# Kernel optimization log

Measured on AMD Instinct MI355X. Metric: run time of the kernel, lower is better.

Reference implementation:

```python
import jax, jax.numpy as jnp
import numpy as np

B, C, H, W = 8, 512, 32, 32
EMB, HEADS, GROUPS = 512, 8, 32
DH = EMB // HEADS
EPS = 1e-5


def setup_inputs() -> dict:
    key = jax.random.key(0)
    ks = jax.random.split(key, 11)
    s_in = 1.0 / np.sqrt(C)
    s_emb = 1.0 / np.sqrt(EMB)
    return {
        "x": jax.random.normal(ks[0], (B, C, H, W), jnp.float32),
        "Wq": jax.random.uniform(ks[1], (C, EMB), jnp.float32, -s_in, s_in),
        "bq": jax.random.uniform(ks[2], (EMB,), jnp.float32, -s_in, s_in),
        "Wk": jax.random.uniform(ks[3], (C, EMB), jnp.float32, -s_in, s_in),
        "bk": jax.random.uniform(ks[4], (EMB,), jnp.float32, -s_in, s_in),
        "Wv": jax.random.uniform(ks[5], (C, EMB), jnp.float32, -s_in, s_in),
        "bv": jax.random.uniform(ks[6], (EMB,), jnp.float32, -s_in, s_in),
        "Wo": jax.random.uniform(ks[7], (EMB, EMB), jnp.float32, -s_emb, s_emb),
        "bo": jax.random.uniform(ks[8], (EMB,), jnp.float32, -s_emb, s_emb),
        "gn_w": jnp.ones((EMB,), jnp.float32),
        "gn_b": jnp.zeros((EMB,), jnp.float32),
    }


def _group_norm(y, w, b):
    # y: [B, C, H, W]; normalize within each of GROUPS channel groups over (C//G, H, W)
    b_, c_, h_, w_ = y.shape
    yg = y.reshape(b_, GROUPS, c_ // GROUPS, h_, w_)
    mean = yg.mean(axis=(2, 3, 4), keepdims=True)
    var = yg.var(axis=(2, 3, 4), keepdims=True)
    yg = (yg - mean) * jax.lax.rsqrt(var + EPS)
    y = yg.reshape(b_, c_, h_, w_)
    return y * w[None, :, None, None] + b[None, :, None, None]


def reference(x, Wq, bq, Wk, bk, Wv, bv, Wo, bo, gn_w, gn_b):
    b, c, h, w = x.shape
    s = h * w
    xs = x.reshape(b, c, s).transpose(0, 2, 1)  # [B, S, C]
    # QKV projections, split into heads: [B, heads, S, dh]
    def heads(t):
        return t.reshape(b, s, HEADS, DH).transpose(0, 2, 1, 3)
    q = heads(xs @ Wq + bq)
    k = heads(xs @ Wk + bk)
    v = heads(xs @ Wv + bv)
    scale = DH ** -0.5
    scores = jnp.einsum('bhqd,bhkd->bhqk', q, k) * scale  # [B, heads, S, S]
    attn = jax.nn.softmax(scores, axis=-1)
    out = jnp.einsum('bhqk,bhkd->bhqd', attn, v)  # [B, heads, S, dh]
    out = out.transpose(0, 2, 1, 3).reshape(b, s, EMB)  # concat heads
    proj = out @ Wo + bo  # [B, S, EMB]
    proj = proj.transpose(0, 2, 1).reshape(b, EMB, h, w)
    return _group_norm(proj + x, gn_w, gn_b)
```

## Files before the change

kernel.cpp:

```cpp
#include <hip/hip_runtime.h>

#define BB 8
#define CC 512
#define SS 1024
#define EMB 512
#define HEADS 8
#define DH 64
#define GROUPS 32
#define CPG 16
#define EPS 1e-5f

typedef __bf16 bf16x8 __attribute__((ext_vector_type(8)));
typedef __bf16 bf16x4 __attribute__((ext_vector_type(4)));
typedef float f32x4 __attribute__((ext_vector_type(4)));
typedef unsigned short u16x4 __attribute__((ext_vector_type(4)));

__device__ inline unsigned short f2bf(float f) {
    union { float f; unsigned u; } c; c.f = f;
    unsigned u = c.u + 0x7FFF + ((c.u >> 16) & 1);
    return (unsigned short)(u >> 16);
}

#if defined(__has_builtin)
#if __has_builtin(__builtin_amdgcn_exp2f)
#define EXP2F(x) __builtin_amdgcn_exp2f(x)
#endif
#endif
#ifndef EXP2F
#define EXP2F(x) __expf(0.69314718f * (x))
#endif

#define MFMA16(a, b, c) __builtin_amdgcn_mfma_f32_16x16x32_bf16((a), (b), (c), 0, 0, 0)
#define GLOAD_LDS16(g, s)                                                     \
    __builtin_amdgcn_global_load_lds(                                         \
        (const __attribute__((address_space(1))) void*)(g),                   \
        (__attribute__((address_space(3))) void*)(s), 16, 0, 0)

__global__ __launch_bounds__(256) void prep_all(
    const float* __restrict__ x,
    const float* __restrict__ Wq, const float* __restrict__ Wk,
    const float* __restrict__ Wv, const float* __restrict__ Wo,
    unsigned short* __restrict__ xT, unsigned short* __restrict__ Wt)
{
    __shared__ float tile[32][33];
    const int t = threadIdx.x;

    if (blockIdx.x < 4096) {
        const int i  = blockIdx.x;
        const int s0 = (i & 31) * 32;
        const int c0 = ((i >> 5) & 15) * 32;
        const int b  = i >> 9;
        {
            int c = t >> 3, s4 = (t & 7) * 4;
            float4 v = *(const float4*)(x + ((size_t)b * CC + c0 + c) * SS + s0 + s4);
            tile[c][s4] = v.x; tile[c][s4 + 1] = v.y;
            tile[c][s4 + 2] = v.z; tile[c][s4 + 3] = v.w;
        }
        __syncthreads();
        {
            int sr = t >> 3, c4 = (t & 7) * 4;
            u16x4 o;
            #pragma unroll
            for (int i2 = 0; i2 < 4; ++i2) o[i2] = f2bf(tile[c4 + i2][sr]);
            *(u16x4*)(xT + ((size_t)(b << 10) + s0 + sr) * CC + c0 + c4) = o;
        }
    } else {
        const int i  = blockIdx.x - 4096;
        const int k0 = (i & 15) * 32;
        const int n0 = ((i >> 4) & 15) * 32;
        const int z  = i >> 8;
        const float* W = (z == 0) ? Wq : (z == 1) ? Wk : (z == 2) ? Wv : Wo;
        unsigned short* dst = Wt + (size_t)z * EMB * CC;
        {
            int k = t >> 3, n4 = (t & 7) * 4;
            float4 v = *(const float4*)(W + (size_t)(k0 + k) * EMB + n0 + n4);
            tile[k][n4] = v.x; tile[k][n4 + 1] = v.y;
            tile[k][n4 + 2] = v.z; tile[k][n4 + 3] = v.w;
        }
        __syncthreads();
        {
            int n = t >> 3, k4 = (t & 7) * 4;
            u16x4 o;
            #pragma unroll
            for (int i2 = 0; i2 < 4; ++i2) o[i2] = f2bf(tile[k4 + i2][n]);
            *(u16x4*)(dst + (size_t)(n0 + n) * CC + k0 + k4) = o;
        }
    }
}

#define GEMM_CORE(Aptr, Bptr)                                                  \
    __shared__ __align__(16) char lds[32768];                                  \
    const int t = threadIdx.x, w = t >> 6, l = t & 63;                         \
    const int wr = w >> 1, wc = w & 1;                                         \
    const int rl = l & 15, kh = l >> 4;                                        \
    f32x4 acc[4][4] = {};                                                      \
    {                                                                          \
        const int srow = w * 32 + (l >> 2);                                    \
        const int sslot = (l & 3) ^ ((srow >> 1) & 3);                         \
        const char* Ag0 = (const char*)(Aptr) + (size_t)(m0 + srow) * 1024 + sslot * 16;      \
        const char* Ag1 = (const char*)(Aptr) + (size_t)(m0 + srow + 16) * 1024 + (((l & 3) ^ (((srow + 16) >> 1) & 3)) * 16); \
        const char* Bg0 = (const char*)(Bptr) + (size_t)(n0 + srow) * 1024 + sslot * 16;      \
        const char* Bg1 = (const char*)(Bptr) + (size_t)(n0 + srow + 16) * 1024 + (((l & 3) ^ (((srow + 16) >> 1) & 3)) * 16); \
        for (int kt = 0; kt < 16; ++kt) {                                      \
            if (kt == 0) {                                                     \
                GLOAD_LDS16(Ag0, lds + w * 2048);                              \
                GLOAD_LDS16(Ag1, lds + w * 2048 + 1024);                       \
                GLOAD_LDS16(Bg0, lds + 8192 + w * 2048);                       \
                GLOAD_LDS16(Bg1, lds + 8192 + w * 2048 + 1024);                \
                __syncthreads();                                               \
            }                                                                  \
            const int buf = kt & 1;                                            \
            if (kt < 15) {                                                     \
                const int kb = (kt + 1) * 64;                                  \
                char* Al = lds + (buf ^ 1) * 16384;                            \
                char* Bl = Al + 8192;                                          \
                GLOAD_LDS16(Ag0 + kb, Al + w * 2048);                          \
                GLOAD_LDS16(Ag1 + kb, Al + w * 2048 + 1024);                   \
                GLOAD_LDS16(Bg0 + kb, Bl + w * 2048);                          \
                GLOAD_LDS16(Bg1 + kb, Bl + w * 2048 + 1024);                   \
            }                                                                  \
            const char* Al = lds + buf * 16384;                                \
            const char* Bl = Al + 8192;                                        \
            bf16x8 af[4], bfr[4];                                              \
            _Pragma("unroll")                                                  \
            for (int i = 0; i < 4; ++i) {                                      \
                int row = wr * 64 + i * 16 + rl;                               \
                af[i] = *(const bf16x8*)(Al + row * 64 + ((kh ^ ((row >> 1) & 3)) << 4)); \
                int col = wc * 64 + i * 16 + rl;                               \
                bfr[i] = *(const bf16x8*)(Bl + col * 64 + ((kh ^ ((col >> 1) & 3)) << 4)); \
            }                                                                  \
            _Pragma("unroll")                                                  \
            for (int i = 0; i < 4; ++i)                                        \
                _Pragma("unroll")                                              \
                for (int j = 0; j < 4; ++j)                                    \
                    acc[i][j] = MFMA16(af[i], bfr[j], acc[i][j]);              \
            __syncthreads();                                                   \
        }                                                                      \
    }

__global__ __launch_bounds__(256) void qkv_mm(
    const unsigned short* __restrict__ xT, const unsigned short* __restrict__ Wt,
    const float* __restrict__ bq, const float* __restrict__ bk,
    const float* __restrict__ bv,
    unsigned short* __restrict__ Qb, unsigned short* __restrict__ Kb,
    unsigned short* __restrict__ Vb)
{
    const int z = blockIdx.z;
    const unsigned short* Bt = Wt + (size_t)z * EMB * CC;
    const float* bias = (z == 0) ? bq : (z == 1) ? bk : bv;
    const int m0 = blockIdx.x * 128, n0 = blockIdx.y * 128;

    GEMM_CORE(xT, Bt)

    if (z == 2) {
        #pragma unroll
        for (int i = 0; i < 4; ++i) {
            #pragma unroll
            for (int j = 0; j < 4; ++j) {
                int n = n0 + wc * 64 + j * 16 + rl;
                int h = n >> 6, d = n & 63;
                float bi = bias[n];
                int mb = m0 + wr * 64 + i * 16 + kh * 4;
                int b = mb >> 10, s = mb & 1023;
                bf16x4 o;
                #pragma unroll
                for (int r = 0; r < 4; ++r) o[r] = (__bf16)(acc[i][j][r] + bi);
                *(bf16x4*)((__bf16*)Vb + (((size_t)(b * HEADS + h)) * DH + d) * SS + s) = o;
            }
        }
    } else {
        unsigned short* outp = (z == 0) ? Qb : Kb;
        const float qs = (z == 0) ? 0.1803368801f : 1.0f;
        #pragma unroll
        for (int i = 0; i < 4; ++i) {
            #pragma unroll
            for (int j = 0; j < 4; ++j) {
                int n = n0 + wc * 64 + j * 16 + rl;
                int h = n >> 6, d = n & 63;
                float bi = bias[n];
                #pragma unroll
                for (int r = 0; r < 4; ++r) {
                    int m = m0 + wr * 64 + i * 16 + kh * 4 + r;
                    int b = m >> 10, s = m & 1023;
                    ((__bf16*)outp)[(((size_t)(b * HEADS + h)) * SS + s) * DH + d] =
                        (__bf16)((acc[i][j][r] + bi) * qs);
                }
            }
        }
    }
}

__global__ __launch_bounds__(256) void proj_mm(
    const unsigned short* __restrict__ AO, const unsigned short* __restrict__ Wot,
    const float* __restrict__ bo, const float* __restrict__ x,
    unsigned short* __restrict__ Yb)
{
    const int m0 = blockIdx.x * 128, n0 = blockIdx.y * 128;

    GEMM_CORE(AO, Wot)

    #pragma unroll
    for (int i = 0; i < 4; ++i) {
        #pragma unroll
        for (int j = 0; j < 4; ++j) {
            int n = n0 + wc * 64 + j * 16 + rl;
            float bi = bo[n];
            int mb = m0 + wr * 64 + i * 16 + kh * 4;
            int b = mb >> 10, s = mb & 1023;
            const float4 xr = *(const float4*)(x + ((size_t)b * CC + n) * SS + s);
            bf16x4 o;
            o[0] = (__bf16)(acc[i][j][0] + bi + xr.x);
            o[1] = (__bf16)(acc[i][j][1] + bi + xr.y);
            o[2] = (__bf16)(acc[i][j][2] + bi + xr.z);
            o[3] = (__bf16)(acc[i][j][3] + bi + xr.w);
            *(bf16x4*)((__bf16*)Yb + ((size_t)b * CC + n) * SS + s) = o;
        }
    }
}

__global__ __launch_bounds__(256) void attn_mfma(
    const unsigned short* __restrict__ Q, const unsigned short* __restrict__ K,
    const unsigned short* __restrict__ V, unsigned short* __restrict__ Aout)
{
    __shared__ __align__(16) char lds[49152];

    const int wg  = blockIdx.x;
    const int xcd = wg & 7;
    const int idx = wg >> 3;
    const int pair = xcd * 8 + (idx >> 3);
    const int qb   = idx & 7;
    const int h = pair & 7;
    const int b = pair >> 3;
    const int q0 = qb * 128;

    const size_t kbase = ((size_t)b * HEADS + h) * SS * DH;
    const size_t vbase = ((size_t)b * HEADS + h) * DH * SS;

    const int t  = threadIdx.x;
    const int w  = t >> 6;
    const int l  = t & 63;
    const int g  = l >> 4;
    const int qi = l & 15;
    char* Pl = lds + 32768 + w * 4096;

    bf16x8 qf[2][2];
    #pragma unroll
    for (int u = 0; u < 2; ++u) {
        const unsigned short* qrow =
            Q + kbase + (size_t)(q0 + w * 32 + u * 16 + qi) * DH;
        qf[u][0] = *(const bf16x8*)(qrow + g * 8);
        qf[u][1] = *(const bf16x8*)(qrow + 32 + g * 8);
    }

    const int srow = t >> 3;
    const int seg  = t & 7;
    const unsigned short* kg0 = K + kbase + (size_t)srow * DH + ((seg ^ (srow & 7)) * 8);
    const unsigned short* vg0 = V + vbase + (size_t)srow * SS + ((seg ^ (srow & 7)) * 8);

#define ATTN_STAGE(bb, ktn)                                                    \
    GLOAD_LDS16(kg0 + (ktn) * 4096, lds + (bb) + t * 16);                      \
    GLOAD_LDS16(kg0 + (ktn) * 4096 + 2048, lds + (bb) + 4096 + t * 16);        \
    GLOAD_LDS16(vg0 + (ktn) * 64, lds + (bb) + 8192 + t * 16);                 \
    GLOAD_LDS16(vg0 + (ktn) * 64 + 32768, lds + (bb) + 12288 + t * 16);

    f32x4 O[4][2] = {};
    float m2[2]   = {-1e30f, -1e30f};
    float lsum[2] = {0.f, 0.f};

    int bufb = 0;
    ATTN_STAGE(0, 0)
    __syncthreads();

    for (int kt = 0; kt < 16; ++kt) {
        if (kt < 15) { ATTN_STAGE(bufb ^ 16384, kt + 1) }

        const char* Kl = lds + bufb;
        const char* Vl = lds + bufb + 8192;

        f32x4 st[4][2] = {};
        __builtin_amdgcn_s_setprio(1);
        #pragma unroll
        for (int tt = 0; tt < 4; ++tt) {
            int row = tt * 16 + qi;
            bf16x8 kf0 = *(const bf16x8*)(Kl + row * 128 +
                          ((g * 16) ^ ((row & 7) << 4)));
            bf16x8 kf1 = *(const bf16x8*)(Kl + row * 128 +
                          ((64 + g * 16) ^ ((row & 7) << 4)));
            #pragma unroll
            for (int u = 0; u < 2; ++u) {
                st[tt][u] = MFMA16(kf0, qf[u][0], st[tt][u]);
                st[tt][u] = MFMA16(kf1, qf[u][1], st[tt][u]);
            }
        }
        __builtin_amdgcn_s_setprio(0);

        float pmax[2] = {-1e30f, -1e30f};
        #pragma unroll
        for (int tt = 0; tt < 4; ++tt)
            #pragma unroll
            for (int u = 0; u < 2; ++u)
                #pragma unroll
                for (int r = 0; r < 4; ++r)
                    pmax[u] = fmaxf(pmax[u], st[tt][u][r]);
        #pragma unroll
        for (int u = 0; u < 2; ++u) {
            if (!__all(pmax[u] <= m2[u] + 8.0f)) {
                float gm = fmaxf(pmax[u], __shfl_xor(pmax[u], 16));
                gm = fmaxf(gm, __shfl_xor(gm, 32));
                float newm = fmaxf(m2[u], gm);
                float alpha = EXP2F(m2[u] - newm);
                #pragma unroll
                for (int dt = 0; dt < 4; ++dt)
                    #pragma unroll
                    for (int r = 0; r < 4; ++r) O[dt][u][r] *= alpha;
                lsum[u] *= alpha;
                m2[u] = newm;
            }
            #pragma unroll
            for (int tt = 0; tt < 4; ++tt) {
                bf16x4 pk;
                #pragma unroll
                for (int r = 0; r < 4; ++r) {
                    float p = EXP2F(st[tt][u][r] - m2[u]);
                    lsum[u] += p;
                    pk[r] = (__bf16)p;
                }
                *(bf16x4*)(Pl + u * 2048 + qi * 128 +
                           ((tt * 32 + g * 8) ^ ((qi & 7) << 4))) = pk;
            }
        }

        bf16x8 pf[2][2];
        #pragma unroll
        for (int u = 0; u < 2; ++u)
            #pragma unroll
            for (int hh = 0; hh < 2; ++hh)
                pf[u][hh] = *(const bf16x8*)(Pl + u * 2048 + qi * 128 +
                             ((hh * 64 + g * 16) ^ ((qi & 7) << 4)));
        __builtin_amdgcn_s_setprio(1);
        #pragma unroll
        for (int dt = 0; dt < 4; ++dt) {
            int d = dt * 16 + qi;
            bf16x8 vf0 = *(const bf16x8*)(Vl + d * 128 + ((g * 16) ^ ((d & 7) << 4)));
            bf16x8 vf1 = *(const bf16x8*)(Vl + d * 128 + ((64 + g * 16) ^ ((d & 7) << 4)));
            #pragma unroll
            for (int u = 0; u < 2; ++u) {
                O[dt][u] = MFMA16(vf0, pf[u][0], O[dt][u]);
                O[dt][u] = MFMA16(vf1, pf[u][1], O[dt][u]);
            }
        }
        __builtin_amdgcn_s_setprio(0);

        __syncthreads();
        bufb ^= 16384;
    }

    #pragma unroll
    for (int u = 0; u < 2; ++u) {
        float ls = lsum[u];
        ls += __shfl_xor(ls, 16);
        ls += __shfl_xor(ls, 32);
        const float inv = __builtin_amdgcn_rcpf(ls);
        unsigned short* orow = Aout +
            ((size_t)b * SS + q0 + w * 32 + u * 16 + qi) * EMB + h * DH;
        #pragma unroll
        for (int dt = 0; dt < 4; ++dt) {
            bf16x4 o;
            #pragma unroll
            for (int r = 0; r < 4; ++r) o[r] = (__bf16)(O[dt][u][r] * inv);
            *(bf16x4*)((__bf16*)orow + dt * 16 + g * 4) = o;
        }
    }
#undef ATTN_STAGE
}

__global__ __launch_bounds__(256) void gnorm3(
    const __bf16* __restrict__ Yb, const float* __restrict__ gw,
    const float* __restrict__ gb, float* __restrict__ out)
{
    __shared__ __align__(16) __bf16 ybuf[CPG * SS];
    __shared__ float red[8];
    __shared__ float stats[2];

    const int grp = blockIdx.x;
    const int b   = blockIdx.y;
    const int t   = threadIdx.x;
    const size_t base = ((size_t)b * CC + grp * CPG) * SS;
    const __bf16* src = Yb + base;

    float sum = 0.f, sq = 0.f;
    #pragma unroll
    for (int i = 0; i < 8; ++i) {
        int off = i * 2048 + t * 8;
        bf16x8 v = *(const bf16x8*)(src + off);
        *(bf16x8*)(ybuf + off) = v;
        #pragma unroll
        for (int j = 0; j < 8; ++j) {
            float f = (float)v[j];
            sum += f; sq += f * f;
        }
    }
    #pragma unroll
    for (int off = 32; off; off >>= 1) {
        sum += __shfl_down(sum, off);
        sq  += __shfl_down(sq, off);
    }
    const int wid = t >> 6;
    if ((t & 63) == 0) { red[wid] = sum; red[4 + wid] = sq; }
    __syncthreads();
    if (t == 0) {
        float s1 = red[0] + red[1] + red[2] + red[3];
        float s2 = red[4] + red[5] + red[6] + red[7];
        float mean = s1 / (float)(CPG * SS);
        float var  = s2 / (float)(CPG * SS) - mean * mean;
        stats[0] = mean;
        stats[1] = rsqrtf(var + EPS);
    }
    __syncthreads();
    const float mean = stats[0], rs = stats[1];

    #pragma unroll
    for (int i = 0; i < 8; ++i) {
        int off = i * 2048 + t * 8;
        int ch = grp * CPG + (off >> 10);
        float wgt = gw[ch] * rs, bet = gb[ch] - mean * rs * gw[ch];
        bf16x8 v = *(const bf16x8*)(ybuf + off);
        float4 o0, o1;
        o0.x = (float)v[0] * wgt + bet; o0.y = (float)v[1] * wgt + bet;
        o0.z = (float)v[2] * wgt + bet; o0.w = (float)v[3] * wgt + bet;
        o1.x = (float)v[4] * wgt + bet; o1.y = (float)v[5] * wgt + bet;
        o1.z = (float)v[6] * wgt + bet; o1.w = (float)v[7] * wgt + bet;
        *(float4*)(out + base + off)     = o0;
        *(float4*)(out + base + off + 4) = o1;
    }
}

extern "C" void kernel_launch(void* const* d_in, const int* in_sizes, int n_in,
                              void* d_out, int out_size, void* d_ws, size_t ws_size,
                              hipStream_t stream) {
    const float* x   = (const float*)d_in[0];
    const float* Wq  = (const float*)d_in[1];
    const float* bq  = (const float*)d_in[2];
    const float* Wk  = (const float*)d_in[3];
    const float* bk  = (const float*)d_in[4];
    const float* Wv  = (const float*)d_in[5];
    const float* bv  = (const float*)d_in[6];
    const float* Wo  = (const float*)d_in[7];
    const float* bo  = (const float*)d_in[8];
    const float* gnw = (const float*)d_in[9];
    const float* gnb = (const float*)d_in[10];
    float* out = (float*)d_out;
    char* ws  = (char*)d_ws;

    unsigned short* xT  = (unsigned short*)(ws);
    unsigned short* Wt  = (unsigned short*)(ws + 8388608);
    unsigned short* Qb  = (unsigned short*)(ws + 10485760);
    unsigned short* Kb  = (unsigned short*)(ws + 18874368);
    unsigned short* Vb  = (unsigned short*)(ws + 27262976);
    unsigned short* AO  = (unsigned short*)(ws + 35651584);
    unsigned short* Yb  = (unsigned short*)(ws + 44040192);

    prep_all<<<dim3(5120), 256, 0, stream>>>(x, Wq, Wk, Wv, Wo, xT, Wt);
    qkv_mm<<<dim3(64, 4, 3), 256, 0, stream>>>(xT, Wt, bq, bk, bv, Qb, Kb, Vb);
    attn_mfma<<<dim3(512), 256, 0, stream>>>(Qb, Kb, Vb, AO);
    proj_mm<<<dim3(64, 4), 256, 0, stream>>>(AO, Wt + (size_t)3 * EMB * CC, bo, x, Yb);
    gnorm3<<<dim3(32, 8), 256, 0, stream>>>((const __bf16*)Yb, gnw, gnb, out);
}
```

Measured before the change: 83.18 us.

## Load K/V fragments directly from global memory and halve attention query tile

The attention kernel drops its double-buffered LDS staging of K and V tiles and block-wide barriers. Each wave now loads its K and V MFMA fragments straight from global memory, leaving LDS only for the per-wave P tile. The query tile per block shrinks from 128 to 64 rows, with 16 per wave, and the grid doubles to 1024 blocks. This cuts LDS use and sync overhead and should raise occupancy, but it loses K/V reuse across waves through LDS, so global and L2 traffic for K/V roughly quadruples and there is no explicit prefetch overlap.

Result: slower. 168.9 us (+103.1%).

```diff
diff --git a/kernel.cpp b/kernel.cpp
--- a/kernel.cpp
+++ b/kernel.cpp
@@ -222,16 +222,16 @@
     const unsigned short* __restrict__ Q, const unsigned short* __restrict__ K,
     const unsigned short* __restrict__ V, unsigned short* __restrict__ Aout)
 {
-    __shared__ __align__(16) char lds[49152];
+    __shared__ __align__(16) char lds[8192];
 
     const int wg  = blockIdx.x;
     const int xcd = wg & 7;
     const int idx = wg >> 3;
-    const int pair = xcd * 8 + (idx >> 3);
-    const int qb   = idx & 7;
+    const int pair = xcd * 8 + (idx >> 4);
+    const int qb   = idx & 15;
     const int h = pair & 7;
     const int b = pair >> 3;
-    const int q0 = qb * 128;
+    const int q0 = qb * 64;
 
     const size_t kbase = ((size_t)b * HEADS + h) * SS * DH;
     const size_t vbase = ((size_t)b * HEADS + h) * DH * SS;
@@ -241,137 +241,96 @@
     const int l  = t & 63;
     const int g  = l >> 4;
     const int qi = l & 15;
-    char* Pl = lds + 32768 + w * 4096;
-
-    bf16x8 qf[2][2];
+    char* Pl = lds + w * 2048;
+
+    bf16x8 qf[2];
+    {
+        const unsigned short* qrow = Q + kbase + (size_t)(q0 + w * 16 + qi) * DH;
+        qf[0] = *(const bf16x8*)(qrow + g * 8);
+        qf[1] = *(const bf16x8*)(qrow + 32 + g * 8);
+    }
+
+    f32x4 O[4] = {};
+    float m2 = -1e30f, lsum = 0.f;
+
+    #pragma unroll 1
+    for (int kt = 0; kt < 16; ++kt) {
+        const unsigned short* kp = K + kbase + (size_t)(kt * 64 + qi) * DH + g * 8;
+        bf16x8 kf[4][2];
+        #pragma unroll
+        for (int tt = 0; tt < 4; ++tt) {
+            kf[tt][0] = *(const bf16x8*)(kp + tt * 16 * DH);
+            kf[tt][1] = *(const bf16x8*)(kp + tt * 16 * DH + 32);
+        }
+        const unsigned short* vp = V + vbase + (size_t)qi * SS + kt * 64 + g * 8;
+        bf16x8 vf[4][2];
+        #pragma unroll
+        for (int dt = 0; dt < 4; ++dt) {
+            vf[dt][0] = *(const bf16x8*)(vp + (size_t)(dt * 16) * SS);
+            vf[dt][1] = *(const bf16x8*)(vp + (size_t)(dt * 16) * SS + 32);
+        }
+
+        f32x4 st[4] = {};
+        __builtin_amdgcn_s_setprio(1);
+        #pragma unroll
+        for (int tt = 0; tt < 4; ++tt) {
+            st[tt] = MFMA16(kf[tt][0], qf[0], st[tt]);
+            st[tt] = MFMA16(kf[tt][1], qf[1], st[tt]);
+        }
+        __builtin_amdgcn_s_setprio(0);
+
+        float pmax = -1e30f;
+        #pragma unroll
+        for (int tt = 0; tt < 4; ++tt)
+            #pragma unroll
+            for (int r = 0; r < 4; ++r)
+                pmax = fmaxf(pmax, st[tt][r]);
+        if (!__all(pmax <= m2 + 8.0f)) {
+            float gm = fmaxf(pmax, __shfl_xor(pmax, 16));
+            gm = fmaxf(gm, __shfl_xor(gm, 32));
+            float newm = fmaxf(m2, gm);
+            float alpha = EXP2F(m2 - newm);
+            #pragma unroll
+            for (int dt = 0; dt < 4; ++dt)
+                #pragma unroll
+                for (int r = 0; r < 4; ++r) O[dt][r] *= alpha;
+            lsum *= alpha;
+            m2 = newm;
+        }
+        #pragma unroll
+        for (int tt = 0; tt < 4; ++tt) {
+            bf16x4 pk;
+            #pragma unroll
+            for (int r = 0; r < 4; ++r) {
+                float p = EXP2F(st[tt][r] - m2);
+                lsum += p;
+                pk[r] = (__bf16)p;
+            }
+            *(bf16x4*)(Pl + qi * 128 + ((tt * 32 + g * 8) ^ ((qi & 7) << 4))) = pk;
+        }
+
+        bf16x8 pf0 = *(const bf16x8*)(Pl + qi * 128 + ((g * 16) ^ ((qi & 7) << 4)));
+        bf16x8 pf1 = *(const bf16x8*)(Pl + qi * 128 + ((64 + g * 16) ^ ((qi & 7) << 4)));
+        __builtin_amdgcn_s_setprio(1);
+        #pragma unroll
+        for (int dt = 0; dt < 4; ++dt) {
+            O[dt] = MFMA16(vf[dt][0], pf0, O[dt]);
+            O[dt] = MFMA16(vf[dt][1], pf1, O[dt]);
+        }
+        __builtin_amdgcn_s_setprio(0);
+    }
+
+    lsum += __shfl_xor(lsum, 16);
+    lsum += __shfl_xor(lsum, 32);
+    const float inv = __builtin_amdgcn_rcpf(lsum);
+    unsigned short* orow = Aout + ((size_t)b * SS + q0 + w * 16 + qi) * EMB + h * DH;
     #pragma unroll
-    for (int u = 0; u < 2; ++u) {
-        const unsigned short* qrow =
-            Q + kbase + (size_t)(q0 + w * 32 + u * 16 + qi) * DH;
-        qf[u][0] = *(const bf16x8*)(qrow + g * 8);
-        qf[u][1] = *(const bf16x8*)(qrow + 32 + g * 8);
-    }
-
-    const int srow = t >> 3;
-    const int seg  = t & 7;
-    const unsigned short* kg0 = K + kbase + (size_t)srow * DH + ((seg ^ (srow & 7)) * 8);
-    const unsigned short* vg0 = V + vbase + (size_t)srow * SS + ((seg ^ (srow & 7)) * 8);
-
-#define ATTN_STAGE(bb, ktn)                                                    \
-    GLOAD_LDS16(kg0 + (ktn) * 4096, lds + (bb) + t * 16);                      \
-    GLOAD_LDS16(kg0 + (ktn) * 4096 + 2048, lds + (bb) + 4096 + t * 16);        \
-    GLOAD_LDS16(vg0 + (ktn) * 64, lds + (bb) + 8192 + t * 16);                 \
-    GLOAD_LDS16(vg0 + (ktn) * 64 + 32768, lds + (bb) + 12288 + t * 16);
-
-    f32x4 O[4][2] = {};
-    float m2[2]   = {-1e30f, -1e30f};
-    float lsum[2] = {0.f, 0.f};
-
-    int bufb = 0;
-    ATTN_STAGE(0, 0)
-    __syncthreads();
-
-    for (int kt = 0; kt < 16; ++kt) {
-        if (kt < 15) { ATTN_STAGE(bufb ^ 16384, kt + 1) }
-
-        const char* Kl = lds + bufb;
-        const char* Vl = lds + bufb + 8192;
-
-        f32x4 st[4][2] = {};
-        __builtin_amdgcn_s_setprio(1);
-        #pragma unroll
-        for (int tt = 0; tt < 4; ++tt) {
-            int row = tt * 16 + qi;
-            bf16x8 kf0 = *(const bf16x8*)(Kl + row * 128 +
-                          ((g * 16) ^ ((row & 7) << 4)));
-            bf16x8 kf1 = *(const bf16x8*)(Kl + row * 128 +
-                          ((64 + g * 16) ^ ((row & 7) << 4)));
-            #pragma unroll
-            for (int u = 0; u < 2; ++u) {
-                st[tt][u] = MFMA16(kf0, qf[u][0], st[tt][u]);
-                st[tt][u] = MFMA16(kf1, qf[u][1], st[tt][u]);
-            }
-        }
-        __builtin_amdgcn_s_setprio(0);
-
-        float pmax[2] = {-1e30f, -1e30f};
-        #pragma unroll
-        for (int tt = 0; tt < 4; ++tt)
-            #pragma unroll
-            for (int u = 0; u < 2; ++u)
-                #pragma unroll
-                for (int r = 0; r < 4; ++r)
-                    pmax[u] = fmaxf(pmax[u], st[tt][u][r]);
-        #pragma unroll
-        for (int u = 0; u < 2; ++u) {
-            if (!__all(pmax[u] <= m2[u] + 8.0f)) {
-                float gm = fmaxf(pmax[u], __shfl_xor(pmax[u], 16));
-                gm = fmaxf(gm, __shfl_xor(gm, 32));
-                float newm = fmaxf(m2[u], gm);
-                float alpha = EXP2F(m2[u] - newm);
-                #pragma unroll
-                for (int dt = 0; dt < 4; ++dt)
-                    #pragma unroll
-                    for (int r = 0; r < 4; ++r) O[dt][u][r] *= alpha;
-                lsum[u] *= alpha;
-                m2[u] = newm;
-            }
-            #pragma unroll
-            for (int tt = 0; tt < 4; ++tt) {
-                bf16x4 pk;
-                #pragma unroll
-                for (int r = 0; r < 4; ++r) {
-                    float p = EXP2F(st[tt][u][r] - m2[u]);
-                    lsum[u] += p;
-                    pk[r] = (__bf16)p;
-                }
-                *(bf16x4*)(Pl + u * 2048 + qi * 128 +
-                           ((tt * 32 + g * 8) ^ ((qi & 7) << 4))) = pk;
-            }
-        }
-
-        bf16x8 pf[2][2];
-        #pragma unroll
-        for (int u = 0; u < 2; ++u)
-            #pragma unroll
-            for (int hh = 0; hh < 2; ++hh)
-                pf[u][hh] = *(const bf16x8*)(Pl + u * 2048 + qi * 128 +
-                             ((hh * 64 + g * 16) ^ ((qi & 7) << 4)));
-        __builtin_amdgcn_s_setprio(1);
-        #pragma unroll
-        for (int dt = 0; dt < 4; ++dt) {
-            int d = dt * 16 + qi;
-            bf16x8 vf0 = *(const bf16x8*)(Vl + d * 128 + ((g * 16) ^ ((d & 7) << 4)));
-            bf16x8 vf1 = *(const bf16x8*)(Vl + d * 128 + ((64 + g * 16) ^ ((d & 7) << 4)));
-            #pragma unroll
-            for (int u = 0; u < 2; ++u) {
-                O[dt][u] = MFMA16(vf0, pf[u][0], O[dt][u]);
-                O[dt][u] = MFMA16(vf1, pf[u][1], O[dt][u]);
-            }
-        }
-        __builtin_amdgcn_s_setprio(0);
-
-        __syncthreads();
-        bufb ^= 16384;
-    }
-
-    #pragma unroll
-    for (int u = 0; u < 2; ++u) {
-        float ls = lsum[u];
-        ls += __shfl_xor(ls, 16);
-        ls += __shfl_xor(ls, 32);
-        const float inv = __builtin_amdgcn_rcpf(ls);
-        unsigned short* orow = Aout +
-            ((size_t)b * SS + q0 + w * 32 + u * 16 + qi) * EMB + h * DH;
-        #pragma unroll
-        for (int dt = 0; dt < 4; ++dt) {
-            bf16x4 o;
-            #pragma unroll
-            for (int r = 0; r < 4; ++r) o[r] = (__bf16)(O[dt][u][r] * inv);
-            *(bf16x4*)((__bf16*)orow + dt * 16 + g * 4) = o;
-        }
-    }
-#undef ATTN_STAGE
+    for (int dt = 0; dt < 4; ++dt) {
+        bf16x4 o;
+        #pragma unroll
+        for (int r = 0; r < 4; ++r) o[r] = (__bf16)(O[dt][r] * inv);
+        *(bf16x4*)((__bf16*)orow + dt * 16 + g * 4) = o;
+    }
 }
 
 __global__ __launch_bounds__(256) void gnorm3(
@@ -462,7 +421,7 @@
 
     prep_all<<<dim3(5120), 256, 0, stream>>>(x, Wq, Wk, Wv, Wo, xT, Wt);
     qkv_mm<<<dim3(64, 4, 3), 256, 0, stream>>>(xT, Wt, bq, bk, bv, Qb, Kb, Vb);
-    attn_mfma<<<dim3(512), 256, 0, stream>>>(Qb, Kb, Vb, AO);
+    attn_mfma<<<dim3(1024), 256, 0, stream>>>(Qb, Kb, Vb, AO);
     proj_mm<<<dim3(64, 4), 256, 0, stream>>>(AO, Wt + (size_t)3 * EMB * CC, bo, x, Yb);
     gnorm3<<<dim3(32, 8), 256, 0, stream>>>((const __bf16*)Yb, gnw, gnb, out);
 }
```

## Load K fragments directly into registers and keep only V in LDS

Applied to the files above, without the earlier changes.

The attention kernel no longer stages K tiles through shared memory. Each lane reads its K MFMA fragments straight from global memory into double-buffered register arrays, while V keeps its double-buffered LDS staging. The loop is unrolled by two to alternate register buffers, and the row-max and row-sum reductions are reassociated into trees. This cuts LDS use from 48KB to 32KB, which may allow more resident workgroups, and removes the K LDS reads. The cost is higher register pressure and uncoalesced, non-async global K loads whose latency has to be hidden by prefetching one tile ahead.

Result: slower. 91.10 us (+9.5%).

```diff
diff --git a/kernel.cpp b/kernel.cpp
--- a/kernel.cpp
+++ b/kernel.cpp
@@ -222,7 +222,7 @@
     const unsigned short* __restrict__ Q, const unsigned short* __restrict__ K,
     const unsigned short* __restrict__ V, unsigned short* __restrict__ Aout)
 {
-    __shared__ __align__(16) char lds[49152];
+    __shared__ __align__(16) char lds[32768];
 
     const int wg  = blockIdx.x;
     const int xcd = wg & 7;
@@ -241,7 +241,7 @@
     const int l  = t & 63;
     const int g  = l >> 4;
     const int qi = l & 15;
-    char* Pl = lds + 32768 + w * 4096;
+    char* Pl = lds + 16384 + w * 4096;
 
     bf16x8 qf[2][2];
     #pragma unroll
@@ -254,105 +254,111 @@
 
     const int srow = t >> 3;
     const int seg  = t & 7;
-    const unsigned short* kg0 = K + kbase + (size_t)srow * DH + ((seg ^ (srow & 7)) * 8);
     const unsigned short* vg0 = V + vbase + (size_t)srow * SS + ((seg ^ (srow & 7)) * 8);
 
-#define ATTN_STAGE(bb, ktn)                                                    \
-    GLOAD_LDS16(kg0 + (ktn) * 4096, lds + (bb) + t * 16);                      \
-    GLOAD_LDS16(kg0 + (ktn) * 4096 + 2048, lds + (bb) + 4096 + t * 16);        \
-    GLOAD_LDS16(vg0 + (ktn) * 64, lds + (bb) + 8192 + t * 16);                 \
-    GLOAD_LDS16(vg0 + (ktn) * 64 + 32768, lds + (bb) + 12288 + t * 16);
+    const unsigned short* kg = K + kbase + (size_t)qi * DH + g * 8;
+
+#define STAGE_V(bb, ktn)                                                       \
+    GLOAD_LDS16(vg0 + (ktn) * 64, lds + (bb) + t * 16);                        \
+    GLOAD_LDS16(vg0 + (ktn) * 64 + 32 * SS, lds + (bb) + 4096 + t * 16);
+
+#define LOAD_K(dst, ktn)                                                       \
+    _Pragma("unroll")                                                          \
+    for (int tt = 0; tt < 4; ++tt) {                                           \
+        const unsigned short* kp = kg + (size_t)((ktn) * 64 + tt * 16) * DH;   \
+        dst[tt][0] = *(const bf16x8*)(kp);                                     \
+        dst[tt][1] = *(const bf16x8*)(kp + 32);                                \
+    }
 
     f32x4 O[4][2] = {};
     float m2[2]   = {-1e30f, -1e30f};
     float lsum[2] = {0.f, 0.f};
 
-    int bufb = 0;
-    ATTN_STAGE(0, 0)
+    bf16x8 kfA[4][2], kfB[4][2];
+    LOAD_K(kfA, 0)
+    STAGE_V(0, 0)
     __syncthreads();
 
-    for (int kt = 0; kt < 16; ++kt) {
-        if (kt < 15) { ATTN_STAGE(bufb ^ 16384, kt + 1) }
-
-        const char* Kl = lds + bufb;
-        const char* Vl = lds + bufb + 8192;
-
-        f32x4 st[4][2] = {};
-        __builtin_amdgcn_s_setprio(1);
-        #pragma unroll
-        for (int tt = 0; tt < 4; ++tt) {
-            int row = tt * 16 + qi;
-            bf16x8 kf0 = *(const bf16x8*)(Kl + row * 128 +
-                          ((g * 16) ^ ((row & 7) << 4)));
-            bf16x8 kf1 = *(const bf16x8*)(Kl + row * 128 +
-                          ((64 + g * 16) ^ ((row & 7) << 4)));
-            #pragma unroll
-            for (int u = 0; u < 2; ++u) {
-                st[tt][u] = MFMA16(kf0, qf[u][0], st[tt][u]);
-                st[tt][u] = MFMA16(kf1, qf[u][1], st[tt][u]);
-            }
-        }
-        __builtin_amdgcn_s_setprio(0);
-
-        float pmax[2] = {-1e30f, -1e30f};
-        #pragma unroll
-        for (int tt = 0; tt < 4; ++tt)
-            #pragma unroll
-            for (int u = 0; u < 2; ++u)
-                #pragma unroll
-                for (int r = 0; r < 4; ++r)
-                    pmax[u] = fmaxf(pmax[u], st[tt][u][r]);
-        #pragma unroll
-        for (int u = 0; u < 2; ++u) {
-            if (!__all(pmax[u] <= m2[u] + 8.0f)) {
-                float gm = fmaxf(pmax[u], __shfl_xor(pmax[u], 16));
-                gm = fmaxf(gm, __shfl_xor(gm, 32));
-                float newm = fmaxf(m2[u], gm);
-                float alpha = EXP2F(m2[u] - newm);
-                #pragma unroll
-                for (int dt = 0; dt < 4; ++dt)
-                    #pragma unroll
-                    for (int r = 0; r < 4; ++r) O[dt][u][r] *= alpha;
-                lsum[u] *= alpha;
-                m2[u] = newm;
-            }
-            #pragma unroll
-            for (int tt = 0; tt < 4; ++tt) {
-                bf16x4 pk;
-                #pragma unroll
-                for (int r = 0; r < 4; ++r) {
-                    float p = EXP2F(st[tt][u][r] - m2[u]);
-                    lsum[u] += p;
-                    pk[r] = (__bf16)p;
-                }
-                *(bf16x4*)(Pl + u * 2048 + qi * 128 +
-                           ((tt * 32 + g * 8) ^ ((qi & 7) << 4))) = pk;
-            }
-        }
-
-        bf16x8 pf[2][2];
-        #pragma unroll
-        for (int u = 0; u < 2; ++u)
-            #pragma unroll
-            for (int hh = 0; hh < 2; ++hh)
-                pf[u][hh] = *(const bf16x8*)(Pl + u * 2048 + qi * 128 +
-                             ((hh * 64 + g * 16) ^ ((qi & 7) << 4)));
-        __builtin_amdgcn_s_setprio(1);
-        #pragma unroll
-        for (int dt = 0; dt < 4; ++dt) {
-            int d = dt * 16 + qi;
-            bf16x8 vf0 = *(const bf16x8*)(Vl + d * 128 + ((g * 16) ^ ((d & 7) << 4)));
-            bf16x8 vf1 = *(const bf16x8*)(Vl + d * 128 + ((64 + g * 16) ^ ((d & 7) << 4)));
-            #pragma unroll
-            for (int u = 0; u < 2; ++u) {
-                O[dt][u] = MFMA16(vf0, pf[u][0], O[dt][u]);
-                O[dt][u] = MFMA16(vf1, pf[u][1], O[dt][u]);
-            }
-        }
-        __builtin_amdgcn_s_setprio(0);
-
-        __syncthreads();
-        bufb ^= 16384;
+#define TILE_BODY(kfC, kfN, kt, bb)                                            \
+    {                                                                          \
+        if ((kt) < 15) { LOAD_K(kfN, (kt) + 1) STAGE_V((bb) ^ 8192, (kt) + 1) }\
+        const char* Vl = lds + (bb);                                           \
+        f32x4 st[4][2] = {};                                                   \
+        __builtin_amdgcn_s_setprio(1);                                         \
+        _Pragma("unroll")                                                      \
+        for (int tt = 0; tt < 4; ++tt) {                                       \
+            _Pragma("unroll")                                                  \
+            for (int u = 0; u < 2; ++u) {                                      \
+                st[tt][u] = MFMA16(kfC[tt][0], qf[u][0], st[tt][u]);           \
+                st[tt][u] = MFMA16(kfC[tt][1], qf[u][1], st[tt][u]);           \
+            }                                                                  \
+        }                                                                      \
+        __builtin_amdgcn_s_setprio(0);                                         \
+        _Pragma("unroll")                                                      \
+        for (int u = 0; u < 2; ++u) {                                          \
+            float a0 = fmaxf(fmaxf(st[0][u][0], st[0][u][1]),                  \
+                             fmaxf(st[0][u][2], st[0][u][3]));                 \
+            float a1 = fmaxf(fmaxf(st[1][u][0], st[1][u][1]),                  \
+                             fmaxf(st[1][u][2], st[1][u][3]));                 \
+            float a2 = fmaxf(fmaxf(st[2][u][0], st[2][u][1]),                  \
+                             fmaxf(st[2][u][2], st[2][u][3]));                 \
+            float a3 = fmaxf(fmaxf(st[3][u][0], st[3][u][1]),                  \
+                             fmaxf(st[3][u][2], st[3][u][3]));                 \
+            float pmax = fmaxf(fmaxf(a0, a1), fmaxf(a2, a3));                  \
+            if (!__all(pmax <= m2[u] + 8.0f)) {                                \
+                float gm = fmaxf(pmax, __shfl_xor(pmax, 16));                  \
+                gm = fmaxf(gm, __shfl_xor(gm, 32));                            \
+                float newm = fmaxf(m2[u], gm);                                 \
+                float alpha = EXP2F(m2[u] - newm);                             \
+                _Pragma("unroll")                                              \
+                for (int dt = 0; dt < 4; ++dt)                                 \
+                    _Pragma("unroll")                                          \
+                    for (int r = 0; r < 4; ++r) O[dt][u][r] *= alpha;          \
+                lsum[u] *= alpha;                                              \
+                m2[u] = newm;                                                  \
+            }                                                                  \
+            float tl[4];                                                       \
+            _Pragma("unroll")                                                  \
+            for (int tt = 0; tt < 4; ++tt) {                                   \
+                bf16x4 pk;                                                     \
+                float p0 = EXP2F(st[tt][u][0] - m2[u]);                        \
+                float p1 = EXP2F(st[tt][u][1] - m2[u]);                        \
+                float p2 = EXP2F(st[tt][u][2] - m2[u]);                        \
+                float p3 = EXP2F(st[tt][u][3] - m2[u]);                        \
+                pk[0] = (__bf16)p0; pk[1] = (__bf16)p1;                        \
+                pk[2] = (__bf16)p2; pk[3] = (__bf16)p3;                        \
+                tl[tt] = (p0 + p1) + (p2 + p3);                                \
+                *(bf16x4*)(Pl + u * 2048 + qi * 128 +                          \
+                           ((tt * 32 + g * 8) ^ ((qi & 7) << 4))) = pk;        \
+            }                                                                  \
+            lsum[u] += (tl[0] + tl[1]) + (tl[2] + tl[3]);                      \
+        }                                                                      \
+        bf16x8 pf[2][2];                                                       \
+        _Pragma("unroll")                                                      \
+        for (int u = 0; u < 2; ++u)                                            \
+            _Pragma("unroll")                                                  \
+            for (int hh = 0; hh < 2; ++hh)                                     \
+                pf[u][hh] = *(const bf16x8*)(Pl + u * 2048 + qi * 128 +        \
+                             ((hh * 64 + g * 16) ^ ((qi & 7) << 4)));          \
+        __builtin_amdgcn_s_setprio(1);                                         \
+        _Pragma("unroll")                                                      \
+        for (int dt = 0; dt < 4; ++dt) {                                       \
+            int d = dt * 16 + qi;                                              \
+            bf16x8 vf0 = *(const bf16x8*)(Vl + d * 128 + ((g * 16) ^ ((d & 7) << 4)));       \
+            bf16x8 vf1 = *(const bf16x8*)(Vl + d * 128 + ((64 + g * 16) ^ ((d & 7) << 4)));  \
+            _Pragma("unroll")                                                  \
+            for (int u = 0; u < 2; ++u) {                                      \
+                O[dt][u] = MFMA16(vf0, pf[u][0], O[dt][u]);                    \
+                O[dt][u] = MFMA16(vf1, pf[u][1], O[dt][u]);                    \
+            }                                                                  \
+        }                                                                      \
+        __builtin_amdgcn_s_setprio(0);                                         \
+        __syncthreads();                                                       \
+    }
+
+    for (int kt = 0; kt < 16; kt += 2) {
+        TILE_BODY(kfA, kfB, kt, 0)
+        TILE_BODY(kfB, kfA, kt + 1, 8192)
     }
 
     #pragma unroll
@@ -371,7 +377,9 @@
             *(bf16x4*)((__bf16*)orow + dt * 16 + g * 4) = o;
         }
     }
-#undef ATTN_STAGE
+#undef TILE_BODY
+#undef STAGE_V
+#undef LOAD_K
 }
 
 __global__ __launch_bounds__(256) void gnorm3(
```
